# Optimization experiments

Measured on AMD Instinct MI355X. Metric: run time of the kernel, lower is better.

The kernel has to match this reference:

```python
import jax, jax.numpy as jnp
import numpy as np

N_NODES = 100000
N_EDGES = 3200000
NFEAT, HID, NCLASS = 256, 32, 16


def setup_inputs() -> dict:
    key = jax.random.key(0)
    ks = jax.random.split(key, 6)
    x = jax.random.normal(ks[0], (N_NODES, NFEAT), dtype=jnp.float32)
    edge_index = jax.random.randint(ks[1], (2, N_EDGES), 0, N_NODES, dtype=jnp.int64)
    edge_weight = jax.random.uniform(ks[2], (N_EDGES,), dtype=jnp.float32)
    # Glorot-ish init for the two GCNConv linear weights; bias zeros (PyG default init zeros bias)
    W1 = jax.random.normal(ks[3], (NFEAT, HID), dtype=jnp.float32) * (1.0 / np.sqrt(NFEAT))
    b1 = jnp.zeros((HID,), dtype=jnp.float32)
    W2 = jax.random.normal(ks[4], (HID, NCLASS), dtype=jnp.float32) * (1.0 / np.sqrt(HID))
    b2 = jnp.zeros((NCLASS,), dtype=jnp.float32)
    return {"x": x, "edge_index": edge_index, "edge_weight": edge_weight,
            "W1": W1, "b1": b1, "W2": W2, "b2": b2}


def _gcn_norm(row, col, w, n):
    """PyG gcn_norm: add self-loops (weight 1), symmetric normalization."""
    loop = jnp.arange(n, dtype=row.dtype)
    row = jnp.concatenate([row, loop])
    col = jnp.concatenate([col, loop])
    w = jnp.concatenate([w, jnp.ones((n,), dtype=w.dtype)])
    deg = jax.ops.segment_sum(w, col, num_segments=n)  # degree at target nodes
    dinv = jnp.where(deg > 0, jax.lax.rsqrt(deg), 0.0)
    norm = dinv[row] * w * dinv[col]
    return row, col, norm


def _gcn_conv(x, W, b, row, col, norm, n):
    xw = x @ W                                  # [N, out]
    msg = xw[row] * norm[:, None]               # gather at source + scale
    out = jax.ops.segment_sum(msg, col, num_segments=n)  # scatter-add at target
    return out + b


def reference(x, edge_index, edge_weight, W1, b1, W2, b2):
    n = x.shape[0]
    row, col, norm = _gcn_norm(edge_index[0], edge_index[1], edge_weight, n)
    h = jax.nn.relu(_gcn_conv(x, W1, b1, row, col, norm, n))
    # dropout is identity in eval mode
    logits = _gcn_conv(h, W2, b2, row, col, norm, n)
    return jax.nn.log_softmax(logits, axis=1)
```

## Files before the change

### kernel.cpp

```cpp
#include <hip/hip_runtime.h>

#define N_NODES 100000
#define N_EDGES 3200000
#define NFEAT 256
#define HID 32
#define NCLASS 16

#define NB 32
#define CHUNK (N_EDGES / NB)
#define RN 16384
#define NR ((N_NODES + RN - 1) / RN)

#define SCAN_TPB 256
#define SCAN_EPB 1024
#define SCAN_NBLK ((N_NODES + SCAN_EPB - 1) / SCAN_EPB)

#define XPAD 261

__global__ __launch_bounds__(1024) void k_count(const int* __restrict__ col,
                                                unsigned* __restrict__ H) {
    __shared__ unsigned hist[RN];
    int t = threadIdx.x, b = blockIdx.x, r = blockIdx.y;
    int base = r * RN;
    const int* cc = col + (size_t)b * CHUNK;
    for (int i = t; i < RN; i += 1024) hist[i] = 0;
    __syncthreads();
    for (int i = t; i < CHUNK; i += 1024) {
        unsigned d = (unsigned)cc[i] - (unsigned)base;
        if (d < RN) atomicAdd(&hist[d], 1u);
    }
    __syncthreads();
    int lim = min(RN, N_NODES - base);
    unsigned* Hb = H + (size_t)b * N_NODES;
    for (int i = t; i < lim; i += 1024) Hb[base + i] = hist[i];
}

__global__ void k_rowsum(const unsigned* __restrict__ H, int* __restrict__ cnt) {
    int n = blockIdx.x * 256 + threadIdx.x;
    if (n >= N_NODES) return;
    unsigned s = 0;
    #pragma unroll 8
    for (int b = 0; b < NB; ++b) s += H[(size_t)b * N_NODES + n];
    cnt[n] = (int)s;
}

__global__ __launch_bounds__(SCAN_TPB) void k_scanA(const int* __restrict__ cnt,
                                                    int* __restrict__ offs,
                                                    int* __restrict__ bsum) {
    __shared__ int s[SCAN_TPB];
    int t = threadIdx.x;
    int base = blockIdx.x * SCAN_EPB + t * 4;
    int v0 = (base + 0 < N_NODES) ? cnt[base + 0] : 0;
    int v1 = (base + 1 < N_NODES) ? cnt[base + 1] : 0;
    int v2 = (base + 2 < N_NODES) ? cnt[base + 2] : 0;
    int v3 = (base + 3 < N_NODES) ? cnt[base + 3] : 0;
    int sum = v0 + v1 + v2 + v3;
    s[t] = sum;
    __syncthreads();
    for (int off = 1; off < SCAN_TPB; off <<= 1) {
        int x = (t >= off) ? s[t - off] : 0;
        __syncthreads();
        s[t] += x;
        __syncthreads();
    }
    int excl = s[t] - sum;
    if (t == SCAN_TPB - 1) bsum[blockIdx.x] = s[t];
    int run = excl;
    if (base + 0 < N_NODES) offs[base + 0] = run; run += v0;
    if (base + 1 < N_NODES) offs[base + 1] = run; run += v1;
    if (base + 2 < N_NODES) offs[base + 2] = run; run += v2;
    if (base + 3 < N_NODES) offs[base + 3] = run;
}

__global__ __launch_bounds__(128) void k_scanB(int* __restrict__ bsum) {
    __shared__ int s[128];
    int t = threadIdx.x;
    int v = (t < SCAN_NBLK) ? bsum[t] : 0;
    s[t] = v;
    __syncthreads();
    for (int off = 1; off < 128; off <<= 1) {
        int x = (t >= off) ? s[t - off] : 0;
        __syncthreads();
        s[t] += x;
        __syncthreads();
    }
    if (t < SCAN_NBLK) bsum[t] = s[t] - v;
}

__global__ __launch_bounds__(SCAN_TPB) void k_scanC(int* __restrict__ offs,
                                                    const int* __restrict__ bsum) {
    int t = threadIdx.x;
    int add = bsum[blockIdx.x];
    int base = blockIdx.x * SCAN_EPB + t * 4;
    #pragma unroll
    for (int i = 0; i < 4; ++i) {
        int idx = base + i;
        if (idx < N_NODES) offs[idx] += add;
    }
    if (blockIdx.x == 0 && t == 0) offs[N_NODES] = N_EDGES;
}

__global__ void k_bprefix(unsigned* __restrict__ H, const int* __restrict__ offs) {
    int n = blockIdx.x * 256 + threadIdx.x;
    if (n >= N_NODES) return;
    unsigned run = (unsigned)offs[n];
    for (int b = 0; b < NB; ++b) {
        size_t idx = (size_t)b * N_NODES + n;
        unsigned v = H[idx];
        H[idx] = run;
        run += v;
    }
}

__global__ __launch_bounds__(1024) void k_place(const int* __restrict__ col,
                                                const unsigned* __restrict__ B,
                                                unsigned* __restrict__ perm) {
    __shared__ unsigned rk[RN];
    int t = threadIdx.x, b = blockIdx.x, r = blockIdx.y;
    int base = r * RN;
    size_t eb = (size_t)b * CHUNK;
    const unsigned* Bb = B + (size_t)b * N_NODES;
    for (int i = t; i < RN; i += 1024) rk[i] = 0;
    __syncthreads();
    for (int i = t; i < CHUNK; i += 1024) {
        int c = col[eb + i];
        unsigned d = (unsigned)c - (unsigned)base;
        if (d < RN) {
            unsigned rr = atomicAdd(&rk[d], 1u);
            perm[eb + i] = Bb[c] + rr;
        }
    }
}

__global__ void k_emit(const int* __restrict__ row, const float* __restrict__ w,
                       const unsigned* __restrict__ perm, float2* __restrict__ ein) {
    int e = blockIdx.x * 256 + threadIdx.x;
    if (e < N_EDGES) ein[perm[e]] = make_float2(__int_as_float(row[e]), w[e]);
}

__global__ void k_deg(const float2* __restrict__ ein, const int* __restrict__ offs,
                      float* __restrict__ dinv) {
    int idx = blockIdx.x * 256 + threadIdx.x;
    int n = idx >> 2, l = idx & 3;
    if (n >= N_NODES) return;
    int s = offs[n], e = offs[n + 1];
    float sum = 0.f;
    for (int p = s + l; p < e; p += 4) sum += ein[p].y;
    sum += __shfl_xor(sum, 1, 4);
    sum += __shfl_xor(sum, 2, 4);
    if (l == 0) dinv[n] = rsqrtf(1.0f + sum);
}

__global__ void k_norm(float2* __restrict__ ein, const int* __restrict__ offs,
                       const float* __restrict__ dinv) {
    int idx = blockIdx.x * 256 + threadIdx.x;
    int n = idx >> 2, l = idx & 3;
    if (n >= N_NODES) return;
    float dn = dinv[n];
    int s = offs[n], e = offs[n + 1];
    for (int p = s + l; p < e; p += 4) {
        float2 v = ein[p];
        int src = __float_as_int(v.x);
        ein[p].y = dn * dinv[src] * v.y;
    }
}

__global__ __launch_bounds__(256) void k_gemm1s(const float* __restrict__ x,
                                                const float* __restrict__ W1,
                                                float* __restrict__ xwp) {
    __shared__ float sWc[32 * HID];
    __shared__ float sX[32 * XPAD];
    int t = threadIdx.x;
    long rowbase = (long)blockIdx.x * 256;
    int kbase = blockIdx.y * 128;
    float* xw = xwp + (size_t)blockIdx.y * N_NODES * HID;
    int tr = t >> 3;
    int tc = t & 7;
    float acc[8][4] = {};
    for (int k0 = kbase; k0 < kbase + 128; k0 += 32) {
        *(float4*)&sWc[t * 4] = *(const float4*)&W1[k0 * HID + t * 4];
        #pragma unroll
        for (int p = 0; p < 8; ++p) {
            int rt = (t >> 3) + p * 32;
            int kk = (t & 7) * 4;
            long grow = rowbase + rt;
            float4 v = make_float4(0.f, 0.f, 0.f, 0.f);
            if (grow < N_NODES) v = *(const float4*)&x[grow * NFEAT + k0 + kk];
            sX[(kk + 0) * XPAD + rt] = v.x; sX[(kk + 1) * XPAD + rt] = v.y;
            sX[(kk + 2) * XPAD + rt] = v.z; sX[(kk + 3) * XPAD + rt] = v.w;
        }
        __syncthreads();
        #pragma unroll 8
        for (int kk = 0; kk < 32; ++kk) {
            float xv[8], wv[4];
            *(float4*)&xv[0] = *(float4*)&sX[kk * XPAD + tr * 8];
            *(float4*)&xv[4] = *(float4*)&sX[kk * XPAD + tr * 8 + 4];
            *(float4*)&wv[0] = *(float4*)&sWc[(kk) * HID + tc * 4];
            #pragma unroll
            for (int m = 0; m < 8; ++m)
                #pragma unroll
                for (int n = 0; n < 4; ++n)
                    acc[m][n] = fmaf(xv[m], wv[n], acc[m][n]);
        }
        __syncthreads();
    }
    #pragma unroll
    for (int m = 0; m < 8; ++m) {
        long r = rowbase + tr * 8 + m;
        if (r < N_NODES) {
            float4 o = make_float4(acc[m][0], acc[m][1], acc[m][2], acc[m][3]);
            *(float4*)&xw[r * HID + tc * 4] = o;
        }
    }
}

__global__ void k_comb(float4* __restrict__ p0, const float4* __restrict__ p1) {
    int i = blockIdx.x * 256 + threadIdx.x;
    float4 a = p0[i], b = p1[i];
    a.x += b.x; a.y += b.y; a.z += b.z; a.w += b.w;
    p0[i] = a;
}

__global__ __launch_bounds__(256) void k_gather1(const float* __restrict__ xw,
                                                 const float* __restrict__ dinv,
                                                 const float2* __restrict__ ein,
                                                 const int* __restrict__ offs,
                                                 const float* __restrict__ b1,
                                                 float* __restrict__ h) {
    int idx = blockIdx.x * 256 + threadIdx.x;
    int n = idx >> 3, l = idx & 7;
    int c4 = l * 4;
    float di = dinv[n];
    float4 a = *(const float4*)&xw[(long)n * HID + c4];
    float dd = di * di;
    float4 acc = make_float4(a.x * dd, a.y * dd, a.z * dd, a.w * dd);
    int s = offs[n], e = offs[n + 1];
    for (int p0 = s; p0 < e; p0 += 8) {
        int pl = p0 + l;
        float2 pr = (pl < e) ? ein[pl] : make_float2(__int_as_float(n), 0.f);
        int ri = __float_as_int(pr.x);
        #pragma unroll
        for (int j = 0; j < 8; ++j) {
            int r = __shfl(ri, j, 8);
            float nm = __shfl(pr.y, j, 8);
            float4 xr = *(const float4*)&xw[(long)r * HID + c4];
            acc.x = fmaf(xr.x, nm, acc.x);
            acc.y = fmaf(xr.y, nm, acc.y);
            acc.z = fmaf(xr.z, nm, acc.z);
            acc.w = fmaf(xr.w, nm, acc.w);
        }
    }
    float4 bb = *(const float4*)&b1[c4];
    acc.x = fmaxf(acc.x + bb.x, 0.f);
    acc.y = fmaxf(acc.y + bb.y, 0.f);
    acc.z = fmaxf(acc.z + bb.z, 0.f);
    acc.w = fmaxf(acc.w + bb.w, 0.f);
    *(float4*)&h[(long)n * HID + c4] = acc;
}

__global__ __launch_bounds__(256) void k_gemm2(const float* __restrict__ h,
                                               const float* __restrict__ W2,
                                               float* __restrict__ hw) {
    __shared__ float sH[64][33];
    __shared__ float sW2[HID * NCLASS];
    int t = threadIdx.x;
    if (t < 128) {
        int idx = t * 4;
        *(float4*)&sW2[idx] = *(const float4*)&W2[idx];
    }
    long base = (long)blockIdx.x * 64;
    #pragma unroll
    for (int i = 0; i < 2; ++i) {
        int idx = t + i * 256;
        int rt = idx >> 3, kk = (idx & 7) * 4;
        long gr = base + rt;
        float4 v = make_float4(0.f, 0.f, 0.f, 0.f);
        if (gr < N_NODES) v = *(const float4*)&h[gr * HID + kk];
        sH[rt][kk + 0] = v.x; sH[rt][kk + 1] = v.y;
        sH[rt][kk + 2] = v.z; sH[rt][kk + 3] = v.w;
    }
    __syncthreads();
    int r = t >> 2, c4 = (t & 3) * 4;
    float acc[4] = {};
    #pragma unroll
    for (int k = 0; k < HID; ++k) {
        float hv = sH[r][k];
        float wv[4];
        *(float4*)&wv[0] = *(float4*)&sW2[k * NCLASS + c4];
        #pragma unroll
        for (int n = 0; n < 4; ++n) acc[n] = fmaf(hv, wv[n], acc[n]);
    }
    long gr = base + r;
    if (gr < N_NODES) {
        float4 o = make_float4(acc[0], acc[1], acc[2], acc[3]);
        *(float4*)&hw[gr * NCLASS + c4] = o;
    }
}

__global__ __launch_bounds__(256) void k_gather2(const float* __restrict__ hw,
                                                 const float* __restrict__ dinv,
                                                 const float2* __restrict__ ein,
                                                 const int* __restrict__ offs,
                                                 const float* __restrict__ b2,
                                                 float* __restrict__ out) {
    int idx = blockIdx.x * 256 + threadIdx.x;
    int n = idx >> 2, l = idx & 3;
    if (n >= N_NODES) return;
    int c4 = l * 4;
    float di = dinv[n];
    float4 a = *(const float4*)&hw[(long)n * NCLASS + c4];
    float dd = di * di;
    float4 acc = make_float4(a.x * dd, a.y * dd, a.z * dd, a.w * dd);
    int s = offs[n], e = offs[n + 1];
    for (int p0 = s; p0 < e; p0 += 8) {
        int pl0 = p0 + l, pl1 = p0 + 4 + l;
        float2 pr0 = (pl0 < e) ? ein[pl0] : make_float2(__int_as_float(n), 0.f);
        float2 pr1 = (pl1 < e) ? ein[pl1] : make_float2(__int_as_float(n), 0.f);
        int r0 = __float_as_int(pr0.x), r1 = __float_as_int(pr1.x);
        #pragma unroll
        for (int j = 0; j < 4; ++j) {
            int r = __shfl(r0, j, 4);
            float nm = __shfl(pr0.y, j, 4);
            float4 hr = *(const float4*)&hw[(long)r * NCLASS + c4];
            acc.x = fmaf(hr.x, nm, acc.x);
            acc.y = fmaf(hr.y, nm, acc.y);
            acc.z = fmaf(hr.z, nm, acc.z);
            acc.w = fmaf(hr.w, nm, acc.w);
        }
        #pragma unroll
        for (int j = 0; j < 4; ++j) {
            int r = __shfl(r1, j, 4);
            float nm = __shfl(pr1.y, j, 4);
            float4 hr = *(const float4*)&hw[(long)r * NCLASS + c4];
            acc.x = fmaf(hr.x, nm, acc.x);
            acc.y = fmaf(hr.y, nm, acc.y);
            acc.z = fmaf(hr.z, nm, acc.z);
            acc.w = fmaf(hr.w, nm, acc.w);
        }
    }
    float4 bb = *(const float4*)&b2[c4];
    float vx = acc.x + bb.x, vy = acc.y + bb.y, vz = acc.z + bb.z, vw = acc.w + bb.w;
    float m = fmaxf(fmaxf(vx, vy), fmaxf(vz, vw));
    m = fmaxf(m, __shfl_xor(m, 1, 4));
    m = fmaxf(m, __shfl_xor(m, 2, 4));
    float sum = __expf(vx - m) + __expf(vy - m) + __expf(vz - m) + __expf(vw - m);
    sum += __shfl_xor(sum, 1, 4);
    sum += __shfl_xor(sum, 2, 4);
    float ls = m + __logf(sum);
    float4 o = make_float4(vx - ls, vy - ls, vz - ls, vw - ls);
    *(float4*)&out[(long)n * NCLASS + c4] = o;
}

extern "C" void kernel_launch(void* const* d_in, const int* in_sizes, int n_in,
                              void* d_out, int out_size, void* d_ws, size_t ws_size,
                              hipStream_t stream) {
    const float* x  = (const float*)d_in[0];
    const int*   ei = (const int*)d_in[1];
    const float* w  = (const float*)d_in[2];
    const float* W1 = (const float*)d_in[3];
    const float* b1 = (const float*)d_in[4];
    const float* W2 = (const float*)d_in[5];
    const float* b2 = (const float*)d_in[6];
    float* out = (float*)d_out;

    const int* row = ei;
    const int* col = ei + N_EDGES;

    float* ws = (float*)d_ws;
    float2* ein = (float2*)ws;
    unsigned* H = (unsigned*)(ws + 2 * (size_t)N_EDGES);
    float* xwp = (float*)H;
    float* xw = (float*)H;
    unsigned* perm = (unsigned*)(ws + 2 * (size_t)N_EDGES + (size_t)NB * N_NODES);
    float* h = (float*)perm;
    float* hw = xw;
    float* dinv = ws + 2 * (size_t)N_EDGES + (size_t)NB * N_NODES + N_EDGES;
    int* cnt = (int*)(dinv + N_NODES);
    int* offs = cnt + N_NODES;
    int* bsum = offs + N_NODES + 1;

    const int B = 256;

    k_count<<<dim3(NB, NR), 1024, 0, stream>>>(col, H);
    k_rowsum<<<(N_NODES + B - 1) / B, B, 0, stream>>>(H, cnt);
    k_scanA<<<SCAN_NBLK, SCAN_TPB, 0, stream>>>(cnt, offs, bsum);
    k_scanB<<<1, 128, 0, stream>>>(bsum);
    k_scanC<<<SCAN_NBLK, SCAN_TPB, 0, stream>>>(offs, bsum);
    k_bprefix<<<(N_NODES + B - 1) / B, B, 0, stream>>>(H, offs);
    k_place<<<dim3(NB, NR), 1024, 0, stream>>>(col, H, perm);
    k_emit<<<(N_EDGES + B - 1) / B, B, 0, stream>>>(row, w, perm, ein);

    k_deg<<<(N_NODES * 4 + B - 1) / B, B, 0, stream>>>(ein, offs, dinv);
    k_norm<<<(N_NODES * 4 + B - 1) / B, B, 0, stream>>>(ein, offs, dinv);

    k_gemm1s<<<dim3((N_NODES + 255) / 256, 2), 256, 0, stream>>>(x, W1, xwp);
    k_comb<<<(N_NODES * HID / 4) / B, B, 0, stream>>>((float4*)xw, (const float4*)(xwp + (size_t)N_NODES * HID));
    k_gather1<<<(N_NODES * 8) / B, B, 0, stream>>>(xw, dinv, ein, offs, b1, h);

    k_gemm2<<<(N_NODES + 63) / 64, B, 0, stream>>>(h, W2, hw);
    k_gather2<<<(N_NODES * 4 + B - 1) / B, B, 0, stream>>>(hw, dinv, ein, offs, b2, out);
}
```

Before: 321.8 us.

## Pack 16-bit histogram counters and split GEMM1 K into four partials

The count and place kernels now pack two 16-bit counters per shared word, so each block covers 32768 nodes and only half as many block rows scan the column array. This cuts redundant global reads of col, but the 16-bit counters cap each node's per-chunk count at 65535. GEMM1 is split into four K-slices of 64 with smaller shared tiles, which gives more blocks for occupancy, and a wider combine kernel sums the four partials. The workspace layout moves the partials and h into a separate region so they no longer alias H and perm.

```diff
diff --git a/kernel.cpp b/kernel.cpp
--- a/kernel.cpp
+++ b/kernel.cpp
@@ -8,8 +8,8 @@
 
 #define NB 32
 #define CHUNK (N_EDGES / NB)
-#define RN 16384
-#define NR ((N_NODES + RN - 1) / RN)
+#define RN2 32768
+#define NR2 ((N_NODES + RN2 - 1) / RN2)
 
 #define SCAN_TPB 256
 #define SCAN_EPB 1024
@@ -19,20 +19,21 @@
 
 __global__ __launch_bounds__(1024) void k_count(const int* __restrict__ col,
                                                 unsigned* __restrict__ H) {
-    __shared__ unsigned hist[RN];
+    __shared__ unsigned hist[RN2 / 2];
     int t = threadIdx.x, b = blockIdx.x, r = blockIdx.y;
-    int base = r * RN;
+    int base = r * RN2;
     const int* cc = col + (size_t)b * CHUNK;
-    for (int i = t; i < RN; i += 1024) hist[i] = 0;
+    for (int i = t; i < RN2 / 2; i += 1024) hist[i] = 0;
     __syncthreads();
     for (int i = t; i < CHUNK; i += 1024) {
         unsigned d = (unsigned)cc[i] - (unsigned)base;
-        if (d < RN) atomicAdd(&hist[d], 1u);
-    }
-    __syncthreads();
-    int lim = min(RN, N_NODES - base);
+        if (d < RN2) atomicAdd(&hist[d >> 1], 1u << ((d & 1) * 16));
+    }
+    __syncthreads();
+    int lim = min(RN2, N_NODES - base);
     unsigned* Hb = H + (size_t)b * N_NODES;
-    for (int i = t; i < lim; i += 1024) Hb[base + i] = hist[i];
+    for (int i = t; i < lim; i += 1024)
+        Hb[base + i] = (hist[i >> 1] >> ((i & 1) * 16)) & 0xFFFFu;
 }
 
 __global__ void k_rowsum(const unsigned* __restrict__ H, int* __restrict__ cnt) {
@@ -115,18 +116,19 @@
 __global__ __launch_bounds__(1024) void k_place(const int* __restrict__ col,
                                                 const unsigned* __restrict__ B,
                                                 unsigned* __restrict__ perm) {
-    __shared__ unsigned rk[RN];
+    __shared__ unsigned rk[RN2 / 2];
     int t = threadIdx.x, b = blockIdx.x, r = blockIdx.y;
-    int base = r * RN;
+    int base = r * RN2;
     size_t eb = (size_t)b * CHUNK;
     const unsigned* Bb = B + (size_t)b * N_NODES;
-    for (int i = t; i < RN; i += 1024) rk[i] = 0;
+    for (int i = t; i < RN2 / 2; i += 1024) rk[i] = 0;
     __syncthreads();
     for (int i = t; i < CHUNK; i += 1024) {
         int c = col[eb + i];
         unsigned d = (unsigned)c - (unsigned)base;
-        if (d < RN) {
-            unsigned rr = atomicAdd(&rk[d], 1u);
+        if (d < RN2) {
+            unsigned old = atomicAdd(&rk[d >> 1], 1u << ((d & 1) * 16));
+            unsigned rr = (old >> ((d & 1) * 16)) & 0xFFFFu;
             perm[eb + i] = Bb[c] + rr;
         }
     }
@@ -168,21 +170,21 @@
 __global__ __launch_bounds__(256) void k_gemm1s(const float* __restrict__ x,
                                                 const float* __restrict__ W1,
                                                 float* __restrict__ xwp) {
-    __shared__ float sWc[32 * HID];
-    __shared__ float sX[32 * XPAD];
+    __shared__ float sWc[16 * HID];
+    __shared__ float sX[16 * XPAD];
     int t = threadIdx.x;
     long rowbase = (long)blockIdx.x * 256;
-    int kbase = blockIdx.y * 128;
+    int kbase = blockIdx.y * 64;
     float* xw = xwp + (size_t)blockIdx.y * N_NODES * HID;
     int tr = t >> 3;
     int tc = t & 7;
     float acc[8][4] = {};
-    for (int k0 = kbase; k0 < kbase + 128; k0 += 32) {
-        *(float4*)&sWc[t * 4] = *(const float4*)&W1[k0 * HID + t * 4];
-        #pragma unroll
-        for (int p = 0; p < 8; ++p) {
-            int rt = (t >> 3) + p * 32;
-            int kk = (t & 7) * 4;
+    for (int k0 = kbase; k0 < kbase + 64; k0 += 16) {
+        if (t < 128) *(float4*)&sWc[t * 4] = *(const float4*)&W1[k0 * HID + t * 4];
+        #pragma unroll
+        for (int p = 0; p < 4; ++p) {
+            int rt = (t >> 2) + p * 64;
+            int kk = (t & 3) * 4;
             long grow = rowbase + rt;
             float4 v = make_float4(0.f, 0.f, 0.f, 0.f);
             if (grow < N_NODES) v = *(const float4*)&x[grow * NFEAT + k0 + kk];
@@ -190,12 +192,12 @@
             sX[(kk + 2) * XPAD + rt] = v.z; sX[(kk + 3) * XPAD + rt] = v.w;
         }
         __syncthreads();
-        #pragma unroll 8
-        for (int kk = 0; kk < 32; ++kk) {
+        #pragma unroll
+        for (int kk = 0; kk < 16; ++kk) {
             float xv[8], wv[4];
             *(float4*)&xv[0] = *(float4*)&sX[kk * XPAD + tr * 8];
             *(float4*)&xv[4] = *(float4*)&sX[kk * XPAD + tr * 8 + 4];
-            *(float4*)&wv[0] = *(float4*)&sWc[(kk) * HID + tc * 4];
+            *(float4*)&wv[0] = *(float4*)&sWc[kk * HID + tc * 4];
             #pragma unroll
             for (int m = 0; m < 8; ++m)
                 #pragma unroll
@@ -214,10 +216,14 @@
     }
 }
 
-__global__ void k_comb(float4* __restrict__ p0, const float4* __restrict__ p1) {
+__global__ void k_comb(float4* __restrict__ p0, const float4* __restrict__ p1,
+                       const float4* __restrict__ p2, const float4* __restrict__ p3) {
     int i = blockIdx.x * 256 + threadIdx.x;
-    float4 a = p0[i], b = p1[i];
-    a.x += b.x; a.y += b.y; a.z += b.z; a.w += b.w;
+    float4 a = p0[i], b = p1[i], c = p2[i], d = p3[i];
+    a.x += b.x + c.x + d.x;
+    a.y += b.y + c.y + d.y;
+    a.z += b.z + c.z + d.z;
+    a.w += b.w + c.w + d.w;
     p0[i] = a;
 }
 
@@ -369,32 +375,39 @@
     float* ws = (float*)d_ws;
     float2* ein = (float2*)ws;
     unsigned* H = (unsigned*)(ws + 2 * (size_t)N_EDGES);
-    float* xwp = (float*)H;
-    float* xw = (float*)H;
     unsigned* perm = (unsigned*)(ws + 2 * (size_t)N_EDGES + (size_t)NB * N_NODES);
-    float* h = (float*)perm;
-    float* hw = xw;
     float* dinv = ws + 2 * (size_t)N_EDGES + (size_t)NB * N_NODES + N_EDGES;
     int* cnt = (int*)(dinv + N_NODES);
     int* offs = cnt + N_NODES;
     int* bsum = offs + N_NODES + 1;
+    size_t xwp_off = (size_t)(2 * (size_t)N_EDGES + (size_t)NB * N_NODES + N_EDGES
+                              + 3 * N_NODES + 1 + 128);
+    xwp_off = (xwp_off + 3) & ~(size_t)3;
+    float* xwp = ws + xwp_off;
+    float* xw = xwp;
+    float* hw = xwp + (size_t)N_NODES * HID;
+    float* h = xwp + 4 * (size_t)N_NODES * HID;
 
     const int B = 256;
 
-    k_count<<<dim3(NB, NR), 1024, 0, stream>>>(col, H);
+    k_count<<<dim3(NB, NR2), 1024, 0, stream>>>(col, H);
     k_rowsum<<<(N_NODES + B - 1) / B, B, 0, stream>>>(H, cnt);
     k_scanA<<<SCAN_NBLK, SCAN_TPB, 0, stream>>>(cnt, offs, bsum);
     k_scanB<<<1, 128, 0, stream>>>(bsum);
     k_scanC<<<SCAN_NBLK, SCAN_TPB, 0, stream>>>(offs, bsum);
     k_bprefix<<<(N_NODES + B - 1) / B, B, 0, stream>>>(H, offs);
-    k_place<<<dim3(NB, NR), 1024, 0, stream>>>(col, H, perm);
+    k_place<<<dim3(NB, NR2), 1024, 0, stream>>>(col, H, perm);
     k_emit<<<(N_EDGES + B - 1) / B, B, 0, stream>>>(row, w, perm, ein);
 
     k_deg<<<(N_NODES * 4 + B - 1) / B, B, 0, stream>>>(ein, offs, dinv);
     k_norm<<<(N_NODES * 4 + B - 1) / B, B, 0, stream>>>(ein, offs, dinv);
 
-    k_gemm1s<<<dim3((N_NODES + 255) / 256, 2), 256, 0, stream>>>(x, W1, xwp);
-    k_comb<<<(N_NODES * HID / 4) / B, B, 0, stream>>>((float4*)xw, (const float4*)(xwp + (size_t)N_NODES * HID));
+    k_gemm1s<<<dim3((N_NODES + 255) / 256, 4), 256, 0, stream>>>(x, W1, xwp);
+    k_comb<<<(N_NODES * HID / 4) / B, B, 0, stream>>>(
+        (float4*)xw,
+        (const float4*)(xwp + 1 * (size_t)N_NODES * HID),
+        (const float4*)(xwp + 2 * (size_t)N_NODES * HID),
+        (const float4*)(xwp + 3 * (size_t)N_NODES * HID));
     k_gather1<<<(N_NODES * 8) / B, B, 0, stream>>>(xw, dinv, ein, offs, b1, h);
 
     k_gemm2<<<(N_NODES + 63) / 64, B, 0, stream>>>(h, W2, hw);
```

Result: slower. 398.7 us (+23.9%).
